# Kernel tuning notes

Measured on AMD Instinct MI355X. Metric: run time of the kernel, lower is better.

The kernel has to match this reference:

```python
import jax, jax.numpy as jnp
import numpy as np

N_NODES, N_EDGES, CH, FEAT = 20000, 320000, 256, 118


def setup_inputs() -> dict:
    key = jax.random.key(0)
    ks = jax.random.split(key, 8)
    x = jax.random.uniform(ks[0], (N_NODES, FEAT), dtype=jnp.float32)
    edge_index = jax.random.randint(ks[1], (2, N_EDGES), 0, N_NODES, dtype=jnp.int64)
    s = 0.05
    W_embed = jax.random.normal(ks[2], (FEAT, CH), dtype=jnp.float32) * s
    b_embed = jnp.zeros((CH,), jnp.float32)
    W1 = jax.random.normal(ks[3], (CH, CH), dtype=jnp.float32) * s
    b1 = jnp.zeros((CH,), jnp.float32)
    W2 = jax.random.normal(ks[4], (CH, CH), dtype=jnp.float32) * s
    b2 = jnp.zeros((CH,), jnp.float32)
    return {"x": x, "edge_index": edge_index, "W_embed": W_embed, "b_embed": b_embed,
            "W1": W1, "b1": b1, "W2": W2, "b2": b2}


def reference(x, edge_index, W_embed, b_embed, W1, b1, W2, b2):
    n = x.shape[0]
    # node embedding: Linear(118 -> C)
    h = x @ W_embed + b_embed  # [N, C]
    src, dst = edge_index[0], edge_index[1]
    # message: gather x_j per edge, dense1 + exact GELU (dropout = identity in eval)
    msg = jax.nn.gelu(h[src] @ W1 + b1, approximate=False)  # [E, C]
    # mean aggregation into destination nodes
    agg = jax.ops.segment_sum(msg, dst, num_segments=n)  # [N, C]
    cnt = jax.ops.segment_sum(jnp.ones((msg.shape[0],), msg.dtype), dst, num_segments=n)
    agg = agg / jnp.maximum(cnt, 1.0)[:, None]
    # update: dense2 + exact GELU
    out = jax.nn.gelu(agg @ W2 + b2, approximate=False)  # [N, C]
    # final mean over channel dim
    return out.mean(axis=1)  # [N]
```

## Files before the change

kernel.cpp:

```cpp
#include <hip/hip_runtime.h>
#include <math.h>

#define N_NODES 20000
#define N_EDGES 320000
#define CH      256
#define FEAT    118
#define CAP     48

typedef float    f32x4 __attribute__((ext_vector_type(4)));
typedef short    s16x8 __attribute__((ext_vector_type(8)));
typedef _Float16 f16x4 __attribute__((ext_vector_type(4)));
typedef _Float16 f16x8 __attribute__((ext_vector_type(8)));
typedef unsigned short u16;

union Frag  { s16x8 v; u16 u[8]; };
union FragH { f16x8 v; _Float16 h[8]; };

__device__ __forceinline__ float gelu_exact(float x) {
    return 0.5f * x * (1.0f + erff(x * 0.70710678118654752f));
}
__device__ __forceinline__ u16 f2bf(float f) {
    unsigned u = __float_as_uint(f);
    u = (u + 0x7FFFu + ((u >> 16) & 1u)) >> 16;
    return (u16)u;
}
__device__ __forceinline__ float bf2f(u16 h) { return __uint_as_float(((unsigned)h) << 16); }

__global__ __launch_bounds__(256) void prep(const float* __restrict__ x,
                                            const int* __restrict__ ei,
                                            const float* __restrict__ We,
                                            const float* __restrict__ be,
                                            const float* __restrict__ W1,
                                            const float* __restrict__ b1,
                                            const float* __restrict__ W2,
                                            u16* __restrict__ xh, u16* __restrict__ xl,
                                            int* __restrict__ cnt, int* __restrict__ bins,
                                            _Float16* __restrict__ w2h, _Float16* __restrict__ w2l,
                                            u16* __restrict__ wch, u16* __restrict__ wcl,
                                            float* __restrict__ bc) {
    const int b = blockIdx.x, tid = threadIdx.x;
    if (b < 1250) {
        __shared__ float xs[16][132];
        {
            int r = tid >> 4, ci = tid & 15;
            const float* xrow = x + (size_t)(b * 16 + r) * FEAT;
            #pragma unroll
            for (int it = 0; it < 8; it++) {
                int col = ci + it * 16;
                xs[r][col] = (col < FEAT) ? xrow[col] : 0.0f;
            }
        }
        __syncthreads();
        int lane = tid & 63, ks = tid >> 6;
        int row = lane & 15, k0 = ks * 32 + (lane >> 4) * 8;
        Frag hi, lo;
        #pragma unroll
        for (int j = 0; j < 8; j++) {
            float v = xs[row][k0 + j];
            u16 h = f2bf(v);
            hi.u[j] = h; lo.u[j] = f2bf(v - bf2f(h));
        }
        size_t fid = (size_t)b * 256 + tid;
        ((s16x8*)xh)[fid] = hi.v;
        ((s16x8*)xl)[fid] = lo.v;
    } else if (b < 2500) {
        int e = (b - 1250) * 256 + tid;
        int s = ei[e];
        int d = ei[N_EDGES + e];
        int p = atomicAdd(&cnt[d], 1);
        if (p < CAP) bins[(size_t)d * CAP + p] = s;
    } else if (b < 2532) {
        int fid = (b - 2500) * 256 + tid;
        int lane = fid & 63, ks = (fid >> 6) & 7, nt = fid >> 9;
        int n = nt * 16 + (lane & 15);
        int k0 = ks * 32 + (lane >> 4) * 8;
        FragH hi, lo;
        #pragma unroll
        for (int j = 0; j < 8; j++) {
            float v = W2[(size_t)(k0 + j) * 256 + n];
            _Float16 h = (_Float16)v;
            hi.h[j] = h;
            lo.h[j] = (_Float16)((v - (float)h) * 4096.0f);
        }
        ((f16x8*)w2h)[fid] = hi.v;
        ((f16x8*)w2l)[fid] = lo.v;
    } else {
        int f = b - 2532;
        int n = tid;
        if (f < 128) {
            float acc = 0.0f;
            if (f < FEAT) {
                const float* wr = We + (size_t)f * 256;
                #pragma unroll 8
                for (int c = 0; c < 256; c++) acc += wr[c] * W1[(size_t)c * 256 + n];
            }
            int nt = n >> 4, lm = n & 15, ks = f >> 5, q = (f >> 3) & 3, j = f & 7;
            size_t idx = (((size_t)nt * 4 + ks) * 64 + q * 16 + lm) * 8 + j;
            u16 h = f2bf(acc);
            wch[idx] = h;
            wcl[idx] = f2bf(acc - bf2f(h));
        } else {
            float acc = b1[n];
            #pragma unroll 8
            for (int c = 0; c < 256; c++) acc += be[c] * W1[(size_t)c * 256 + n];
            bc[n] = acc;
        }
    }
}

__global__ __launch_bounds__(256) void gemm_main(const u16* __restrict__ Ah_, const u16* __restrict__ Al_,
                                                 const u16* __restrict__ Bh_, const u16* __restrict__ Bl_,
                                                 const float* __restrict__ bias,
                                                 _Float16* __restrict__ Mout) {
    __shared__ _Float16 Ls[16][256];
    const int tid = threadIdx.x, wave = tid >> 6, lane = tid & 63;
    const int quad = lane >> 4, lm = lane & 15;
    const int mt = blockIdx.x, nt0 = wave * 4;
    const s16x8* Ah = (const s16x8*)Ah_; const s16x8* Al = (const s16x8*)Al_;
    const s16x8* Bh = (const s16x8*)Bh_; const s16x8* Bl = (const s16x8*)Bl_;
    f32x4 acc[4] = {f32x4{0,0,0,0}, f32x4{0,0,0,0}, f32x4{0,0,0,0}, f32x4{0,0,0,0}};
    #pragma unroll
    for (int ks = 0; ks < 4; ks++) {
        s16x8 a_h = Ah[((size_t)mt * 4 + ks) * 64 + lane];
        s16x8 a_l = Al[((size_t)mt * 4 + ks) * 64 + lane];
        #pragma unroll
        for (int t = 0; t < 4; t++) {
            s16x8 bh = Bh[((size_t)(nt0 + t) * 4 + ks) * 64 + lane];
            s16x8 bl = Bl[((size_t)(nt0 + t) * 4 + ks) * 64 + lane];
            acc[t] = __builtin_amdgcn_mfma_f32_16x16x32_bf16(a_h, bh, acc[t], 0, 0, 0);
            acc[t] = __builtin_amdgcn_mfma_f32_16x16x32_bf16(a_l, bh, acc[t], 0, 0, 0);
            acc[t] = __builtin_amdgcn_mfma_f32_16x16x32_bf16(a_h, bl, acc[t], 0, 0, 0);
        }
    }
    #pragma unroll
    for (int t = 0; t < 4; t++) {
        float bn = bias[(nt0 + t) * 16 + lm];
        #pragma unroll
        for (int r = 0; r < 4; r++)
            Ls[quad * 4 + r][(nt0 + t) * 16 + lm] = (_Float16)gelu_exact(acc[t][r] + bn);
    }
    __syncthreads();
    s16x8* dst = (s16x8*)Mout + (size_t)mt * 512;
    const s16x8* src = (const s16x8*)&Ls[0][0];
    dst[tid]       = src[tid];
    dst[256 + tid] = src[256 + tid];
}

__global__ __launch_bounds__(256) void aggregate(const _Float16* __restrict__ M,
                                                 const int* __restrict__ cnt,
                                                 const int* __restrict__ bins,
                                                 _Float16* __restrict__ aggf) {
    const int sl = blockIdx.x & 7;
    const int wave = threadIdx.x >> 6, lane = threadIdx.x & 63;
    const int node = (blockIdx.x >> 3) * 4 + wave;
    const int esub = lane >> 2, c4 = lane & 3;
    int c = cnt[node];
    int cc = min(c, CAP);
    int myid = (lane < cc) ? bins[(size_t)node * CAP + lane] : 0;
    float a[8] = {0.f, 0.f, 0.f, 0.f, 0.f, 0.f, 0.f, 0.f};
    for (int j = 0; j < cc; j += 16) {
        int e = min(j + esub, cc - 1);
        int s = __shfl(myid, e, 64);
        f16x8 v = *(const f16x8*)(M + (size_t)s * CH + sl * 32 + c4 * 8);
        if (j + esub < cc) {
            #pragma unroll
            for (int q = 0; q < 8; q++) a[q] += (float)v[q];
        }
    }
    #pragma unroll
    for (int off = 4; off < 64; off <<= 1)
        #pragma unroll
        for (int q = 0; q < 8; q++) a[q] += __shfl_xor(a[q], off, 64);
    if (esub == 0) {
        float inv = 1.0f / (float)max(c, 1);
        FragH o;
        #pragma unroll
        for (int q = 0; q < 8; q++) o.h[q] = (_Float16)(a[q] * inv);
        int mt = node >> 4, lm = node & 15;
        size_t base = (((size_t)mt * 8 + sl) * 64 + c4 * 16 + lm) * 8;
        *(f16x8*)(aggf + base) = o.v;
    }
}

__global__ __launch_bounds__(256) void gemm_mean(const _Float16* __restrict__ Af_,
                                                 const _Float16* __restrict__ Bh_, const _Float16* __restrict__ Bl_,
                                                 const float* __restrict__ bias,
                                                 float* __restrict__ out) {
    __shared__ float part[4][32];
    const int tid = threadIdx.x, wave = tid >> 6, lane = tid & 63;
    const int quad = lane >> 4, lm = lane & 15;
    const int mt0 = blockIdx.x * 2, nt0 = wave * 4;
    const f16x8* Af = (const f16x8*)Af_;
    const f16x8* Bh = (const f16x8*)Bh_; const f16x8* Bl = (const f16x8*)Bl_;
    f32x4 acch[2][4], accl[2][4];
    #pragma unroll
    for (int mi = 0; mi < 2; mi++)
        #pragma unroll
        for (int t = 0; t < 4; t++) {
            acch[mi][t] = f32x4{0.f, 0.f, 0.f, 0.f};
            accl[mi][t] = f32x4{0.f, 0.f, 0.f, 0.f};
        }
    #pragma unroll
    for (int ks = 0; ks < 8; ks++) {
        f16x8 a0 = Af[((size_t)(mt0 + 0) * 8 + ks) * 64 + lane];
        f16x8 a1 = Af[((size_t)(mt0 + 1) * 8 + ks) * 64 + lane];
        #pragma unroll
        for (int t = 0; t < 4; t++) {
            f16x8 bh = Bh[((size_t)(nt0 + t) * 8 + ks) * 64 + lane];
            f16x8 bl = Bl[((size_t)(nt0 + t) * 8 + ks) * 64 + lane];
            acch[0][t] = __builtin_amdgcn_mfma_f32_16x16x32_f16(a0, bh, acch[0][t], 0, 0, 0);
            accl[0][t] = __builtin_amdgcn_mfma_f32_16x16x32_f16(a0, bl, accl[0][t], 0, 0, 0);
            acch[1][t] = __builtin_amdgcn_mfma_f32_16x16x32_f16(a1, bh, acch[1][t], 0, 0, 0);
            accl[1][t] = __builtin_amdgcn_mfma_f32_16x16x32_f16(a1, bl, accl[1][t], 0, 0, 0);
        }
    }
    float p[2][4] = {{0.f,0.f,0.f,0.f},{0.f,0.f,0.f,0.f}};
    #pragma unroll
    for (int t = 0; t < 4; t++) {
        float bn = bias[(nt0 + t) * 16 + lm];
        #pragma unroll
        for (int mi = 0; mi < 2; mi++)
            #pragma unroll
            for (int r = 0; r < 4; r++)
                p[mi][r] += gelu_exact(acch[mi][t][r] + accl[mi][t][r] * (1.0f / 4096.0f) + bn);
    }
    #pragma unroll
    for (int off = 1; off < 16; off <<= 1)
        #pragma unroll
        for (int mi = 0; mi < 2; mi++)
            #pragma unroll
            for (int r = 0; r < 4; r++)
                p[mi][r] += __shfl_xor(p[mi][r], off, 64);
    if (lm == 0)
        #pragma unroll
        for (int mi = 0; mi < 2; mi++)
            #pragma unroll
            for (int r = 0; r < 4; r++)
                part[wave][mi * 16 + quad * 4 + r] = p[mi][r];
    __syncthreads();
    if (tid < 32) {
        float s = part[0][tid] + part[1][tid] + part[2][tid] + part[3][tid];
        out[blockIdx.x * 32 + tid] = s * (1.0f / 256.0f);
    }
}

extern "C" void kernel_launch(void* const* d_in, const int* in_sizes, int n_in,
                              void* d_out, int out_size, void* d_ws, size_t ws_size,
                              hipStream_t stream) {
    const float* x  = (const float*)d_in[0];
    const int*   ei = (const int*)d_in[1];
    const float* We = (const float*)d_in[2];
    const float* be = (const float*)d_in[3];
    const float* W1 = (const float*)d_in[4];
    const float* b1 = (const float*)d_in[5];
    const float* W2 = (const float*)d_in[6];
    const float* b2 = (const float*)d_in[7];
    float* out = (float*)d_out;

    char* ws = (char*)d_ws;
    size_t off = 0;
    u16* xh = (u16*)(ws + off);
    _Float16* aggf = (_Float16*)(ws + off);
    off += 5120000;
    u16* xl = (u16*)(ws + off); off += 5120000;
    _Float16* M = (_Float16*)(ws + off); off += 10240000;
    u16* wch = (u16*)(ws + off); off += 65536;
    u16* wcl = (u16*)(ws + off); off += 65536;
    _Float16* w2h = (_Float16*)(ws + off); off += 131072;
    _Float16* w2l = (_Float16*)(ws + off); off += 131072;
    float* bc = (float*)(ws + off); off += 1024;
    int* cnt  = (int*)(ws + off); off += N_NODES * 4;
    int* bins = (int*)(ws + off); off += (size_t)N_NODES * CAP * 4;

    hipMemsetAsync(cnt, 0, N_NODES * sizeof(int), stream);
    prep<<<2661, 256, 0, stream>>>(x, ei, We, be, W1, b1, W2,
                                   xh, xl, cnt, bins, w2h, w2l, wch, wcl, bc);
    gemm_main<<<N_NODES / 16, 256, 0, stream>>>(xh, xl, wch, wcl, bc, M);
    aggregate<<<(N_NODES / 4) * 8, 256, 0, stream>>>(M, cnt, bins, aggf);
    gemm_mean<<<N_NODES / 32, 256, 0, stream>>>(aggf, w2h, w2l, b2, out);
}
```

Baseline: 187.9 us.

## Aggregate full node row per wave with unrolled gathers instead of channel slices

The aggregate kernel now assigns one wave per destination node covering all 256 channels. Each half-wave handles alternating edges, and the kernel issues four 16-byte gathers per lane before accumulating, instead of splitting channels into 8 slices across separate blocks. This cuts the number of blocks, the redundant reads of counts and bin indices, and the cross-lane reduction work, and raises memory-level parallelism per lane. In exchange each wave handles more edges serially, and it uses more registers for the in-flight loads.

```diff
diff --git a/kernel.cpp b/kernel.cpp
--- a/kernel.cpp
+++ b/kernel.cpp
@@ -150,34 +150,39 @@
                                                  const int* __restrict__ cnt,
                                                  const int* __restrict__ bins,
                                                  _Float16* __restrict__ aggf) {
-    const int sl = blockIdx.x & 7;
-    const int wave = threadIdx.x >> 6, lane = threadIdx.x & 63;
-    const int node = (blockIdx.x >> 3) * 4 + wave;
-    const int esub = lane >> 2, c4 = lane & 3;
+    int node = (blockIdx.x * 256 + threadIdx.x) >> 6;
+    int lane = threadIdx.x & 63;
+    int half = lane >> 5, lh = lane & 31;
     int c = cnt[node];
     int cc = min(c, CAP);
     int myid = (lane < cc) ? bins[(size_t)node * CAP + lane] : 0;
     float a[8] = {0.f, 0.f, 0.f, 0.f, 0.f, 0.f, 0.f, 0.f};
-    for (int j = 0; j < cc; j += 16) {
-        int e = min(j + esub, cc - 1);
-        int s = __shfl(myid, e, 64);
-        f16x8 v = *(const f16x8*)(M + (size_t)s * CH + sl * 32 + c4 * 8);
-        if (j + esub < cc) {
-            #pragma unroll
-            for (int q = 0; q < 8; q++) a[q] += (float)v[q];
-        }
-    }
-    #pragma unroll
-    for (int off = 4; off < 64; off <<= 1)
-        #pragma unroll
-        for (int q = 0; q < 8; q++) a[q] += __shfl_xor(a[q], off, 64);
-    if (esub == 0) {
+    for (int j = 0; j < cc; j += 8) {
+        f16x8 v[4];
+        #pragma unroll
+        for (int u = 0; u < 4; u++) {
+            int e = min(j + u * 2 + half, cc - 1);
+            int s = __shfl(myid, e, 64);
+            v[u] = *(const f16x8*)(M + (size_t)s * CH + lh * 8);
+        }
+        #pragma unroll
+        for (int u = 0; u < 4; u++) {
+            if (j + u * 2 + half < cc) {
+                #pragma unroll
+                for (int q = 0; q < 8; q++) a[q] += (float)v[u][q];
+            }
+        }
+    }
+    #pragma unroll
+    for (int q = 0; q < 8; q++) a[q] += __shfl_xor(a[q], 32, 64);
+    if (half == 0) {
         float inv = 1.0f / (float)max(c, 1);
         FragH o;
         #pragma unroll
         for (int q = 0; q < 8; q++) o.h[q] = (_Float16)(a[q] * inv);
         int mt = node >> 4, lm = node & 15;
-        size_t base = (((size_t)mt * 8 + sl) * 64 + c4 * 16 + lm) * 8;
+        int ks = lh >> 2, quad = lh & 3;
+        size_t base = (((size_t)mt * 8 + ks) * 64 + quad * 16 + lm) * 8;
         *(f16x8*)(aggf + base) = o.v;
     }
 }
@@ -276,6 +281,6 @@
     prep<<<2661, 256, 0, stream>>>(x, ei, We, be, W1, b1, W2,
                                    xh, xl, cnt, bins, w2h, w2l, wch, wcl, bc);
     gemm_main<<<N_NODES / 16, 256, 0, stream>>>(xh, xl, wch, wcl, bc, M);
-    aggregate<<<(N_NODES / 4) * 8, 256, 0, stream>>>(M, cnt, bins, aggf);
+    aggregate<<<N_NODES / 4, 256, 0, stream>>>(M, cnt, bins, aggf);
     gemm_mean<<<N_NODES / 32, 256, 0, stream>>>(aggf, w2h, w2l, b2, out);
 }
```

Result: faster. 150.8 us (-19.7%).
